# Optimization experiments

Measured on AMD Instinct MI355X. Metric: run time of the kernel, lower is better.

The kernel has to match this reference:

```python
import jax, jax.numpy as jnp
import numpy as np
import math

HIDDEN = 1024
NUM_HEADS = 16
NUM_GROUPS = 16  # source einsum/rearrange only shape-checks when groups == heads
HEAD_DIM = HIDDEN // NUM_HEADS


def rope(x, base=10000.0):
    # x: [b, s, d]; applied to the FULL hidden vector before head split, as in source.
    # Source rope_fn has a reshape bug; this is the intended rotate-half RoPE with
    # half_d frequencies 1/base^(i/half_d) (== 1/base^(2i/d)).
    b, s, d = x.shape
    half = d // 2
    x1, x2 = x[..., :half], x[..., half:]
    pos = jnp.arange(s, dtype=x.dtype)[:, None]                          # [s,1]
    inv_freq = 1.0 / (base ** (jnp.arange(half, dtype=x.dtype) / half))  # [half]
    ang = pos * inv_freq[None, :]                                        # [s,half]
    sin = jnp.sin(ang)[None]                                             # [1,s,half]
    cos = jnp.cos(ang)[None]
    return jnp.concatenate([x1 * cos - x2 * sin, x2 * cos + x1 * sin], axis=-1)


def setup_inputs() -> dict:
    key = jax.random.key(0)
    ks = jax.random.split(key, 10)
    scale = 1.0 / math.sqrt(HIDDEN)
    inp = {
        "x": jax.random.normal(ks[0], (2, 2048, HIDDEN), dtype=jnp.float32),
        "attn_mask": jax.random.randint(ks[1], (2, 2048), 0, 2, dtype=jnp.int32),
        "Wq": jax.random.uniform(ks[2], (HIDDEN, HIDDEN), jnp.float32, -scale, scale),
        "bq": jax.random.uniform(ks[3], (HIDDEN,), jnp.float32, -scale, scale),
        "Wk": jax.random.uniform(ks[4], (HIDDEN, HIDDEN), jnp.float32, -scale, scale),
        "bk": jax.random.uniform(ks[5], (HIDDEN,), jnp.float32, -scale, scale),
        "Wv": jax.random.uniform(ks[6], (HIDDEN, HIDDEN), jnp.float32, -scale, scale),
        "bv": jax.random.uniform(ks[7], (HIDDEN,), jnp.float32, -scale, scale),
        "Wo": jax.random.uniform(ks[8], (HIDDEN, HIDDEN), jnp.float32, -scale, scale),
        "bo": jax.random.uniform(ks[9], (HIDDEN,), jnp.float32, -scale, scale),
    }
    return inp


def reference(x, attn_mask, Wq, bq, Wk, bk, Wv, bv, Wo, bo):
    b, s, _ = x.shape
    g = NUM_GROUPS
    subh = NUM_HEADS // g  # = 1 here
    d = HIDDEN // g        # per-group dim (== head dim when g == h)

    q = rope(x @ Wq.T + bq)
    k = rope(x @ Wk.T + bk)
    v = x @ Wv.T + bv

    # q: b s (g subh d) -> b g subh s d ; k,v: b s (g d) -> b g s d
    q = q.reshape(b, s, g, subh, d).transpose(0, 2, 3, 1, 4)
    k = k.reshape(b, s, g, d).transpose(0, 2, 1, 3)
    v = v.reshape(b, s, g, d).transpose(0, 2, 1, 3)

    e = jnp.einsum('bghqd,bgkd->bghqk', q, k) / math.sqrt(HEAD_DIM)  # [b,g,subh,s,s]
    mask5 = attn_mask[:, None, None, None, :]  # broadcast over g, subh, query
    e = jnp.where(mask5 == 0, -jnp.inf, e)
    attn = jax.nn.softmax(e, axis=-1)
    out = jnp.einsum('bghqk,bgkd->bghqd', attn, v)            # [b,g,subh,s,d]
    out = out.transpose(0, 3, 1, 2, 4).reshape(b, s, HIDDEN)  # b s (g subh d)
    return out @ Wo.T + bo
```

## Files before the change

kernel.cpp:

```cpp
#include <hip/hip_runtime.h>
#include <hip/hip_bf16.h>


constexpr int Bb  = 2;
constexpr int Ss  = 2048;
constexpr int Hh  = 1024;
constexpr int NHh = 16;
constexpr int Mm  = Bb * Ss;

typedef __attribute__((ext_vector_type(8))) unsigned short ushort8;
typedef __attribute__((ext_vector_type(4))) unsigned short ushort4_t;
typedef __attribute__((ext_vector_type(8))) short short8;
typedef __attribute__((ext_vector_type(4))) float f32x4;

__device__ __forceinline__ unsigned short f2bf(float f) {
    unsigned int u = __float_as_uint(f);
    u += 0x7fffu + ((u >> 16) & 1u);
    return (unsigned short)(u >> 16);
}
__device__ __forceinline__ float bf2f(unsigned short h) {
    return __uint_as_float(((unsigned int)h) << 16);
}
__device__ __forceinline__ void gload16(const void* g, void* l) {
    __builtin_amdgcn_global_load_lds(
        (const __attribute__((address_space(1))) unsigned int*)g,
        (__attribute__((address_space(3))) unsigned int*)l, 16, 0, 0);
}

__global__ __launch_bounds__(256) void convert_k(
    const float* __restrict__ x,
    const float* __restrict__ Wq, const float* __restrict__ Wk,
    const float* __restrict__ Wv, const float* __restrict__ Wo,
    unsigned short* __restrict__ xb, unsigned short* __restrict__ wall)
{
    size_t e = ((size_t)blockIdx.x * 256 + threadIdx.x) << 3;
    const float* s; unsigned short* d;
    if (e < (size_t)Mm * Hh) {
        s = x + e; d = xb + e;
    } else {
        size_t f = e - (size_t)Mm * Hh;
        int t = (int)(f >> 20);
        const float* w = (t == 0) ? Wq : (t == 1) ? Wk : (t == 2) ? Wv : Wo;
        s = w + (f & 1048575);
        d = wall + f;
    }
    float4 a = *(const float4*)s;
    float4 b = *(const float4*)(s + 4);
    ushort8 o;
    o[0] = f2bf(a.x); o[1] = f2bf(a.y); o[2] = f2bf(a.z); o[3] = f2bf(a.w);
    o[4] = f2bf(b.x); o[5] = f2bf(b.y); o[6] = f2bf(b.z); o[7] = f2bf(b.w);
    *(ushort8*)d = o;
}

#define GEMM_BODY(ATYPE_PTR, WPTR, K0MAX)                                          \
    __shared__ unsigned short As[128 * 64];                                        \
    __shared__ unsigned short Bs[128 * 64];                                        \
    const int tid  = threadIdx.x;                                                  \
    const int lane = tid & 63;                                                     \
    const int w    = tid >> 6;                                                     \
    const int wr   = w >> 1, wc = w & 1;                                           \
    const int l16  = lane & 15, g = lane >> 4;                                     \
    const int R0   = blockIdx.x * 128;                                             \
    char* asb = (char*)As; char* bsb = (char*)Bs;                                  \
    f32x4 acc[4][4] = {};                                                          \
    for (int k0 = 0; k0 < K0MAX; k0 += 64) {                                       \
        _Pragma("unroll")                                                          \
        for (int it = 0; it < 4; ++it) {                                           \
            int sbase = w * 4096 + it * 1024;                                      \
            int boff  = sbase + lane * 16;                                         \
            int r     = boff >> 7;                                                 \
            int c     = (boff >> 4) & 7;                                           \
            int col   = k0 + ((c ^ (r & 7)) << 3);                                 \
            gload16(&ATYPE_PTR[(size_t)(R0 + r) * 1024 + col], asb + sbase);       \
            gload16(&WPTR[(size_t)(gn + r) * 1024 + col], bsb + sbase);            \
        }                                                                          \
        __syncthreads();                                                           \
        short8 bfrag[4][2];                                                        \
        _Pragma("unroll")                                                          \
        for (int u = 0; u < 4; ++u) {                                              \
            int row = wc * 64 + u * 16 + l16;                                      \
            _Pragma("unroll")                                                      \
            for (int s = 0; s < 2; ++s)                                            \
                bfrag[u][s] = *(const short8*)(bsb + row * 128 +                   \
                               ((s * 64 + g * 16) ^ ((row & 7) << 4)));            \
        }                                                                          \
        _Pragma("unroll")                                                          \
        for (int t = 0; t < 4; ++t) {                                              \
            int row = wr * 64 + t * 16 + l16;                                      \
            short8 af[2];                                                          \
            _Pragma("unroll")                                                      \
            for (int s = 0; s < 2; ++s)                                            \
                af[s] = *(const short8*)(asb + row * 128 +                         \
                         ((s * 64 + g * 16) ^ ((row & 7) << 4)));                  \
            _Pragma("unroll")                                                      \
            for (int u = 0; u < 4; ++u) {                                          \
                acc[t][u] = __builtin_amdgcn_mfma_f32_16x16x32_bf16(af[0], bfrag[u][0], acc[t][u], 0, 0, 0); \
                acc[t][u] = __builtin_amdgcn_mfma_f32_16x16x32_bf16(af[1], bfrag[u][1], acc[t][u], 0, 0, 0); \
            }                                                                      \
        }                                                                          \
        __syncthreads();                                                           \
    }

__global__ __launch_bounds__(256) void gemm_qkv_k(
    const unsigned short* __restrict__ xb, const unsigned short* __restrict__ wall,
    const float* __restrict__ bq, const float* __restrict__ bk, const float* __restrict__ bv,
    unsigned short* __restrict__ q, unsigned short* __restrict__ k2,
    unsigned short* __restrict__ v)
{
    const int gn = blockIdx.y * 128;
    GEMM_BODY(xb, wall, 1024)

    const int sel = gn >> 10;
    const int n0  = gn & 1023;
    const float* bias = (sel == 0) ? bq : (sel == 1) ? bk : bv;
    unsigned short* outp = (sel == 0) ? q : (sel == 1) ? k2 : v;
    const float qs = (sel == 0) ? 0.18033688011112042f : 1.0f;
    #pragma unroll
    for (int u = 0; u < 4; ++u) {
        int coll = wc * 64 + u * 16 + l16;
        float bb = bias[n0 + coll];
        #pragma unroll
        for (int t = 0; t < 4; ++t)
            #pragma unroll
            for (int rr = 0; rr < 4; ++rr) {
                int row = R0 + wr * 64 + t * 16 + g * 4 + rr;
                outp[(size_t)row * 1024 + n0 + coll] = f2bf((acc[t][u][rr] + bb) * qs);
            }
    }
}

__global__ __launch_bounds__(256) void gemm_out_k(
    const unsigned short* __restrict__ ao, const unsigned short* __restrict__ wo,
    const float* __restrict__ bo, float* __restrict__ out)
{
    const int gn = blockIdx.y * 128;
    GEMM_BODY(ao, wo, 1024)

    #pragma unroll
    for (int u = 0; u < 4; ++u) {
        int coll = wc * 64 + u * 16 + l16;
        float bb = bo[gn + coll];
        #pragma unroll
        for (int t = 0; t < 4; ++t)
            #pragma unroll
            for (int rr = 0; rr < 4; ++rr) {
                int row = R0 + wr * 64 + t * 16 + g * 4 + rr;
                out[(size_t)row * 1024 + gn + coll] = acc[t][u][rr] + bb;
            }
    }
}

__global__ __launch_bounds__(256) void rope_k(
    unsigned short* __restrict__ q, unsigned short* __restrict__ kk)
{
    int idx = blockIdx.x * 256 + threadIdx.x;
    int row = idx >> 7;
    int j4  = (idx & 127) << 2;
    int pos = row & (Ss - 1);
    size_t base = (size_t)row * 1024;

    ushort4_t qa = *(ushort4_t*)&q[base + j4];
    ushort4_t qb = *(ushort4_t*)&q[base + 512 + j4];
    ushort4_t ka = *(ushort4_t*)&kk[base + j4];
    ushort4_t kb = *(ushort4_t*)&kk[base + 512 + j4];

    #pragma unroll
    for (int t = 0; t < 4; ++t) {
        float jj = (float)(j4 + t);
        float inv = exp2f(jj * -0.0259525632621414f);
        float ang = (float)pos * inv;
        float sn, cs;
        __sincosf(ang, &sn, &cs);
        float a = bf2f(qa[t]), b = bf2f(qb[t]);
        qa[t] = f2bf(a * cs - b * sn);
        qb[t] = f2bf(b * cs + a * sn);
        float c = bf2f(ka[t]), d = bf2f(kb[t]);
        ka[t] = f2bf(c * cs - d * sn);
        kb[t] = f2bf(d * cs + c * sn);
    }
    *(ushort4_t*)&q[base + j4]        = qa;
    *(ushort4_t*)&q[base + 512 + j4]  = qb;
    *(ushort4_t*)&kk[base + j4]       = ka;
    *(ushort4_t*)&kk[base + 512 + j4] = kb;
}

__global__ __launch_bounds__(256, 3) void flash_k(
    const unsigned short* __restrict__ q, const unsigned short* __restrict__ k,
    const unsigned short* __restrict__ v, const int* __restrict__ mask,
    unsigned short* __restrict__ ao)
{
    __shared__ unsigned short Ks[2][64 * 64];
    __shared__ unsigned short Vt[2][64 * 72];
    __shared__ unsigned short Pb[4][32 * 64];

    const int F   = blockIdx.x;
    const int xcd = F & 7, j = F >> 3;
    const int grp = xcd * 4 + (j >> 4);
    const int qb  = j & 15;
    const int h   = grp & 15;
    const int bz  = grp >> 4;

    const int tid  = threadIdx.x;
    const int lane = tid & 63;
    const int w    = tid >> 6;
    const int l16  = lane & 15;
    const int g    = lane >> 4;
    const int sw   = (lane & 7) << 4;

    const int qrowbase = bz * Ss + qb * 128 + w * 32;
    const size_t kvbase = (size_t)(bz * Ss) * 1024 + h * 64;

    short8 qf[2][2];
    #pragma unroll
    for (int t = 0; t < 2; ++t)
        #pragma unroll
        for (int s = 0; s < 2; ++s)
            qf[t][s] = *(const short8*)&q[(size_t)(qrowbase + t * 16 + l16) * 1024
                                          + h * 64 + s * 32 + g * 8];

    f32x4 O[2][4];
    #pragma unroll
    for (int t = 0; t < 2; ++t)
        #pragma unroll
        for (int d = 0; d < 4; ++d) O[t][d] = (f32x4)0.f;
    f32x4 Osum[2];
    Osum[0] = (f32x4)0.f; Osum[1] = (f32x4)0.f;
    float mrow[2] = {-1.0e4f, -1.0e4f};

    const float THR = 10.0f;

    short8 ones;
    #pragma unroll
    for (int e = 0; e < 8; ++e) ones[e] = (short)0x3F80;

    const int kv    = lane;
    const int dbase = w * 16;

    ushort8 vr0 = *(const ushort8*)&v[kvbase + (size_t)kv * 1024 + dbase];
    ushort8 vr1 = *(const ushort8*)&v[kvbase + (size_t)kv * 1024 + dbase + 8];
    #pragma unroll
    for (int it = 0; it < 2; ++it) {
        int cid = w * 128 + it * 64 + lane;
        int row = cid >> 3;
        int sub = cid & 7;
        gload16(&k[kvbase + (size_t)row * 1024 + ((sub ^ (row & 7)) << 3)],
                (char*)&Ks[0][0] + w * 2048 + it * 1024);
    }
    #pragma unroll
    for (int jj = 0; jj < 8; ++jj) {
        Vt[0][(dbase + jj) * 72 + kv]     = vr0[jj];
        Vt[0][(dbase + 8 + jj) * 72 + kv] = vr1[jj];
    }
    __syncthreads();

    for (int kt = 0; kt < Ss / 64; ++kt) {
        const int cur = kt & 1;
        char* ksb = (char*)&Ks[cur][0];
        char* vtb = (char*)&Vt[cur][0];
        char* pbb = (char*)&Pb[w][0];
        const bool pre = (kt + 1 < Ss / 64);

        if (pre) {
            size_t nb = kvbase + (size_t)(kt + 1) * 64 * 1024;
            vr0 = *(const ushort8*)&v[nb + (size_t)kv * 1024 + dbase];
            vr1 = *(const ushort8*)&v[nb + (size_t)kv * 1024 + dbase + 8];
            #pragma unroll
            for (int it = 0; it < 2; ++it) {
                int cid = w * 128 + it * 64 + lane;
                int row = cid >> 3;
                int sub = cid & 7;
                gload16(&k[nb + (size_t)row * 1024 + ((sub ^ (row & 7)) << 3)],
                        (char*)&Ks[cur ^ 1][0] + w * 2048 + it * 1024);
            }
        }

        f32x4 S[2][4];
        #pragma unroll
        for (int t = 0; t < 2; ++t)
            #pragma unroll
            for (int kt4 = 0; kt4 < 4; ++kt4) S[t][kt4] = (f32x4)0.f;
        #pragma unroll
        for (int kt4 = 0; kt4 < 4; ++kt4) {
            int key = kt4 * 16 + l16;
            short8 kf0 = *(const short8*)(ksb + key * 128 + ((g * 16) ^ sw));
            short8 kf1 = *(const short8*)(ksb + key * 128 + ((64 + g * 16) ^ sw));
            #pragma unroll
            for (int t = 0; t < 2; ++t) {
                S[t][kt4] = __builtin_amdgcn_mfma_f32_16x16x32_bf16(kf0, qf[t][0], S[t][kt4], 0, 0, 0);
                S[t][kt4] = __builtin_amdgcn_mfma_f32_16x16x32_bf16(kf1, qf[t][1], S[t][kt4], 0, 0, 0);
            }
        }

        int mk[4][4];
        #pragma unroll
        for (int kt4 = 0; kt4 < 4; ++kt4)
            *(int4*)&mk[kt4][0] = *(const int4*)&mask[bz * Ss + kt * 64 + kt4 * 16 + g * 4];
        #pragma unroll
        for (int t = 0; t < 2; ++t)
            #pragma unroll
            for (int kt4 = 0; kt4 < 4; ++kt4)
                #pragma unroll
                for (int r = 0; r < 4; ++r)
                    S[t][kt4][r] = mk[kt4][r] ? S[t][kt4][r] : -1e30f;

        float rm[2];
        #pragma unroll
        for (int t = 0; t < 2; ++t) {
            float m0 = fmaxf(fmaxf(S[t][0][0], S[t][0][1]), fmaxf(S[t][0][2], S[t][0][3]));
            float m1 = fmaxf(fmaxf(S[t][1][0], S[t][1][1]), fmaxf(S[t][1][2], S[t][1][3]));
            float m2 = fmaxf(fmaxf(S[t][2][0], S[t][2][1]), fmaxf(S[t][2][2], S[t][2][3]));
            float m3 = fmaxf(fmaxf(S[t][3][0], S[t][3][1]), fmaxf(S[t][3][2], S[t][3][3]));
            float m  = fmaxf(fmaxf(m0, m1), fmaxf(m2, m3));
            m = fmaxf(m, __shfl_xor(m, 16));
            m = fmaxf(m, __shfl_xor(m, 32));
            rm[t] = m;
        }

        bool grow = (rm[0] > mrow[0] + THR) || (rm[1] > mrow[1] + THR);
        if (__any((int)grow)) {
            float mn0 = fmaxf(mrow[0], rm[0]);
            float mn1 = fmaxf(mrow[1], rm[1]);
            float rs0 = exp2f(mrow[0] - mn0);
            float rs1 = exp2f(mrow[1] - mn1);
            mrow[0] = mn0; mrow[1] = mn1;
            #pragma unroll
            for (int r = 0; r < 4; ++r) {
                float f0 = __shfl(rs0, g * 4 + r);
                float f1 = __shfl(rs1, g * 4 + r);
                #pragma unroll
                for (int dt = 0; dt < 4; ++dt) { O[0][dt][r] *= f0; O[1][dt][r] *= f1; }
                Osum[0][r] *= f0; Osum[1][r] *= f1;
            }
        }

        #pragma unroll
        for (int t = 0; t < 2; ++t) {
            int prow = t * 16 + l16;
            #pragma unroll
            for (int kt4 = 0; kt4 < 4; ++kt4) {
                float p0 = exp2f(S[t][kt4][0] - mrow[t]);
                float p1 = exp2f(S[t][kt4][1] - mrow[t]);
                float p2 = exp2f(S[t][kt4][2] - mrow[t]);
                float p3 = exp2f(S[t][kt4][3] - mrow[t]);
                unsigned int u01, u23;
                asm("v_cvt_pk_bf16_f32 %0, %1, %2" : "=v"(u01) : "v"(p0), "v"(p1));
                asm("v_cvt_pk_bf16_f32 %0, %1, %2" : "=v"(u23) : "v"(p2), "v"(p3));
                int pbyte = (kt4 * 32 + g * 8) ^ sw;
                *(uint2*)(pbb + prow * 128 + pbyte) = make_uint2(u01, u23);
            }
        }

        #pragma unroll
        for (int ks = 0; ks < 2; ++ks) {
            short8 pf[2];
            #pragma unroll
            for (int t = 0; t < 2; ++t)
                pf[t] = *(const short8*)(pbb + (t * 16 + l16) * 128 + ((ks * 64 + g * 16) ^ sw));
            Osum[0] = __builtin_amdgcn_mfma_f32_16x16x32_bf16(pf[0], ones, Osum[0], 0, 0, 0);
            Osum[1] = __builtin_amdgcn_mfma_f32_16x16x32_bf16(pf[1], ones, Osum[1], 0, 0, 0);
            #pragma unroll
            for (int dt = 0; dt < 4; ++dt) {
                short8 vf = *(const short8*)((const char*)vtb
                              + ((dt * 16 + l16) * 72 + ks * 32 + g * 8) * 2);
                O[0][dt] = __builtin_amdgcn_mfma_f32_16x16x32_bf16(pf[0], vf, O[0][dt], 0, 0, 0);
                O[1][dt] = __builtin_amdgcn_mfma_f32_16x16x32_bf16(pf[1], vf, O[1][dt], 0, 0, 0);
            }
        }

        if (pre) {
            #pragma unroll
            for (int jj = 0; jj < 8; ++jj) {
                Vt[cur ^ 1][(dbase + jj) * 72 + kv]     = vr0[jj];
                Vt[cur ^ 1][(dbase + 8 + jj) * 72 + kv] = vr1[jj];
            }
        }
        __syncthreads();
    }

    #pragma unroll
    for (int t = 0; t < 2; ++t)
        #pragma unroll
        for (int r = 0; r < 4; ++r) {
            float inv = 1.0f / Osum[t][r];
            int row = qrowbase + t * 16 + g * 4 + r;
            #pragma unroll
            for (int dt = 0; dt < 4; ++dt)
                ao[(size_t)row * 1024 + h * 64 + dt * 16 + l16] = f2bf(O[t][dt][r] * inv);
        }
}

extern "C" void kernel_launch(void* const* d_in, const int* in_sizes, int n_in,
                              void* d_out, int out_size, void* d_ws, size_t ws_size,
                              hipStream_t stream)
{
    const float* x  = (const float*)d_in[0];
    const int*   am = (const int*)d_in[1];
    const float* Wq = (const float*)d_in[2];
    const float* bq = (const float*)d_in[3];
    const float* Wk = (const float*)d_in[4];
    const float* bk = (const float*)d_in[5];
    const float* Wv = (const float*)d_in[6];
    const float* bv = (const float*)d_in[7];
    const float* Wo = (const float*)d_in[8];
    const float* bo = (const float*)d_in[9];
    float* out = (float*)d_out;

    const size_t NE = (size_t)Mm * Hh;
    unsigned short* q    = (unsigned short*)d_ws;
    unsigned short* k    = q + NE;
    unsigned short* v    = k + NE;
    unsigned short* ao   = v + NE;
    unsigned short* xb   = ao + NE;
    unsigned short* wall = xb + NE;
    unsigned short* wo   = wall + 3u * 1048576u;

    convert_k<<<(2 * NE) / (256 * 8), 256, 0, stream>>>(x, Wq, Wk, Wv, Wo, xb, wall);
    gemm_qkv_k<<<dim3(Mm / 128, 3072 / 128), 256, 0, stream>>>(
        xb, wall, bq, bk, bv, q, k, v);
    rope_k<<<(Mm * 128) / 256, 256, 0, stream>>>(q, k);
    flash_k<<<dim3(Ss / 128 * NHh * Bb), 256, 0, stream>>>(q, k, v, am, ao);
    gemm_out_k<<<dim3(Mm / 128, Hh / 128), 256, 0, stream>>>(ao, wo, bo, out);
}
```

Baseline: 164.4 us.

## Pre-transpose V in a separate kernel and load it async into swizzled LDS

Adds a kernel that writes V transposed per (batch, head) as [d][seq] into workspace. The flash kernel then loads V tiles with async global-to-LDS copies and the same XOR swizzle used for K, replacing the register loads and scalar transposed LDS stores done inside the loop. This is meant to cut per-iteration VALU and LDS store work and shorten the loop's critical path. In exchange it adds a kernel launch and an extra read and write of V through global memory, and it depends on the workspace holding the extra buffer.

```diff
diff --git a/kernel.cpp b/kernel.cpp
--- a/kernel.cpp
+++ b/kernel.cpp
@@ -184,13 +184,37 @@
     *(ushort4_t*)&kk[base + 512 + j4] = kb;
 }
 
+__global__ __launch_bounds__(256) void transpose_v_k(
+    const unsigned short* __restrict__ v, unsigned short* __restrict__ vt)
+{
+    __shared__ unsigned short Ld[64][72];
+    const int bh = blockIdx.y;
+    const int s0 = blockIdx.x * 64;
+    const int bz = bh >> 4, h = bh & 15;
+    const int t  = threadIdx.x;
+    const int r  = t >> 2;
+    const int c0 = (t & 3) * 16;
+
+    const unsigned short* src = &v[(size_t)(bz * Ss + s0 + r) * 1024 + h * 64 + c0];
+    *(ushort8*)&Ld[r][c0]     = *(const ushort8*)src;
+    *(ushort8*)&Ld[r][c0 + 8] = *(const ushort8*)(src + 8);
+    __syncthreads();
+
+    unsigned short* dst = &vt[(size_t)bh * 64 * 2048 + (size_t)r * 2048 + s0 + c0];
+    ushort8 o0, o1;
+    #pragma unroll
+    for (int j = 0; j < 8; ++j) { o0[j] = Ld[c0 + j][r]; o1[j] = Ld[c0 + 8 + j][r]; }
+    *(ushort8*)dst       = o0;
+    *(ushort8*)(dst + 8) = o1;
+}
+
 __global__ __launch_bounds__(256, 3) void flash_k(
     const unsigned short* __restrict__ q, const unsigned short* __restrict__ k,
-    const unsigned short* __restrict__ v, const int* __restrict__ mask,
+    const unsigned short* __restrict__ vt, const int* __restrict__ mask,
     unsigned short* __restrict__ ao)
 {
     __shared__ unsigned short Ks[2][64 * 64];
-    __shared__ unsigned short Vt[2][64 * 72];
+    __shared__ unsigned short Vt[2][64 * 64];
     __shared__ unsigned short Pb[4][32 * 64];
 
     const int F   = blockIdx.x;
@@ -208,7 +232,8 @@
     const int sw   = (lane & 7) << 4;
 
     const int qrowbase = bz * Ss + qb * 128 + w * 32;
-    const size_t kvbase = (size_t)(bz * Ss) * 1024 + h * 64;
+    const size_t kbase  = (size_t)(bz * Ss) * 1024 + h * 64;
+    const size_t vtbase = (size_t)(bz * 16 + h) * 64 * 2048;
 
     short8 qf[2][2];
     #pragma unroll
@@ -233,23 +258,18 @@
     #pragma unroll
     for (int e = 0; e < 8; ++e) ones[e] = (short)0x3F80;
 
-    const int kv    = lane;
-    const int dbase = w * 16;
-
-    ushort8 vr0 = *(const ushort8*)&v[kvbase + (size_t)kv * 1024 + dbase];
-    ushort8 vr1 = *(const ushort8*)&v[kvbase + (size_t)kv * 1024 + dbase + 8];
+    const int cid0 = w * 128 + lane;
+
     #pragma unroll
     for (int it = 0; it < 2; ++it) {
-        int cid = w * 128 + it * 64 + lane;
+        int cid = cid0 + it * 64;
         int row = cid >> 3;
         int sub = cid & 7;
-        gload16(&k[kvbase + (size_t)row * 1024 + ((sub ^ (row & 7)) << 3)],
+        int so  = (sub ^ (row & 7)) << 3;
+        gload16(&k[kbase + (size_t)row * 1024 + so],
                 (char*)&Ks[0][0] + w * 2048 + it * 1024);
-    }
-    #pragma unroll
-    for (int jj = 0; jj < 8; ++jj) {
-        Vt[0][(dbase + jj) * 72 + kv]     = vr0[jj];
-        Vt[0][(dbase + 8 + jj) * 72 + kv] = vr1[jj];
+        gload16(&vt[vtbase + (size_t)row * 2048 + so],
+                (char*)&Vt[0][0] + w * 2048 + it * 1024);
     }
     __syncthreads();
 
@@ -258,19 +278,20 @@
         char* ksb = (char*)&Ks[cur][0];
         char* vtb = (char*)&Vt[cur][0];
         char* pbb = (char*)&Pb[w][0];
-        const bool pre = (kt + 1 < Ss / 64);
-
-        if (pre) {
-            size_t nb = kvbase + (size_t)(kt + 1) * 64 * 1024;
-            vr0 = *(const ushort8*)&v[nb + (size_t)kv * 1024 + dbase];
-            vr1 = *(const ushort8*)&v[nb + (size_t)kv * 1024 + dbase + 8];
+
+        if (kt + 1 < Ss / 64) {
+            size_t knb = kbase + (size_t)(kt + 1) * 64 * 1024;
+            size_t vnb = vtbase + (size_t)(kt + 1) * 64;
             #pragma unroll
             for (int it = 0; it < 2; ++it) {
-                int cid = w * 128 + it * 64 + lane;
+                int cid = cid0 + it * 64;
                 int row = cid >> 3;
                 int sub = cid & 7;
-                gload16(&k[nb + (size_t)row * 1024 + ((sub ^ (row & 7)) << 3)],
+                int so  = (sub ^ (row & 7)) << 3;
+                gload16(&k[knb + (size_t)row * 1024 + so],
                         (char*)&Ks[cur ^ 1][0] + w * 2048 + it * 1024);
+                gload16(&vt[vnb + (size_t)row * 2048 + so],
+                        (char*)&Vt[cur ^ 1][0] + w * 2048 + it * 1024);
             }
         }
 
@@ -360,20 +381,12 @@
             Osum[1] = __builtin_amdgcn_mfma_f32_16x16x32_bf16(pf[1], ones, Osum[1], 0, 0, 0);
             #pragma unroll
             for (int dt = 0; dt < 4; ++dt) {
-                short8 vf = *(const short8*)((const char*)vtb
-                              + ((dt * 16 + l16) * 72 + ks * 32 + g * 8) * 2);
+                short8 vf = *(const short8*)(vtb + (dt * 16 + l16) * 128 + ((ks * 64 + g * 16) ^ sw));
                 O[0][dt] = __builtin_amdgcn_mfma_f32_16x16x32_bf16(pf[0], vf, O[0][dt], 0, 0, 0);
                 O[1][dt] = __builtin_amdgcn_mfma_f32_16x16x32_bf16(pf[1], vf, O[1][dt], 0, 0, 0);
             }
         }
 
-        if (pre) {
-            #pragma unroll
-            for (int jj = 0; jj < 8; ++jj) {
-                Vt[cur ^ 1][(dbase + jj) * 72 + kv]     = vr0[jj];
-                Vt[cur ^ 1][(dbase + 8 + jj) * 72 + kv] = vr1[jj];
-            }
-        }
         __syncthreads();
     }
 
@@ -413,11 +426,13 @@
     unsigned short* xb   = ao + NE;
     unsigned short* wall = xb + NE;
     unsigned short* wo   = wall + 3u * 1048576u;
+    unsigned short* vtg  = wall + 4u * 1048576u;
 
     convert_k<<<(2 * NE) / (256 * 8), 256, 0, stream>>>(x, Wq, Wk, Wv, Wo, xb, wall);
     gemm_qkv_k<<<dim3(Mm / 128, 3072 / 128), 256, 0, stream>>>(
         xb, wall, bq, bk, bv, q, k, v);
     rope_k<<<(Mm * 128) / 256, 256, 0, stream>>>(q, k);
-    flash_k<<<dim3(Ss / 128 * NHh * Bb), 256, 0, stream>>>(q, k, v, am, ao);
+    transpose_v_k<<<dim3(Ss / 64, Bb * NHh), 256, 0, stream>>>(v, vtg);
+    flash_k<<<dim3(Ss / 128 * NHh * Bb), 256, 0, stream>>>(q, k, vtg, am, ao);
     gemm_out_k<<<dim3(Mm / 128, Hh / 128), 256, 0, stream>>>(ao, wo, bo, out);
 }
```

Measured after the change: 165.4 us. No clear change (+0.6%).
